# Optimization experiments

Hardware: AMD Instinct MI355X
Metric: run time of the kernel (lower is better)

## Reference

```python
import jax, jax.numpy as jnp
import numpy as np

K = 64          # number of tags, incl. BOS/EOS
V = 50000       # vocab size (excl. BOS/EOS words)
D = 128         # lexicon embedding dim
BOS_T = K - 2   # BOS tag index
EOS_T = K - 1   # EOS tag index
BATCH = 8192
L = 126         # interior words per sentence (n = L + 2 incl. BOS/EOS)
EPS = 1e-45     # smoothing added to A and B in updateAB


def setup_inputs() -> dict:
    key = jax.random.key(0)
    k1, k2, k3, k4 = jax.random.split(key, 4)
    words = jax.random.randint(k1, (BATCH, L), 0, V, dtype=jnp.int32)
    ThetaB = 0.01 * jax.random.uniform(k2, (K, D), dtype=jnp.float32)
    WA = 0.01 * jax.random.uniform(k3, (K, K), dtype=jnp.float32)
    E = jax.random.normal(k4, (V, D), dtype=jnp.float32)
    return {"words": words, "ThetaB": ThetaB, "WA": WA, "E": E}


def reference(words, ThetaB, WA, E):
    # updateAB(): A = softmax(WA) with BOS column forced to prob 0 (-inf logit)
    WAm = WA.at[:, BOS_T].set(-jnp.inf)
    A = jax.nn.softmax(WAm, axis=1) + EPS                       # [K, K]
    B = jax.nn.softmax(ThetaB @ E.T, axis=1)                    # [K, V]
    B = B.at[EOS_T, :].set(0.0).at[BOS_T, :].set(0.0) + EPS
    logA = jnp.log(A)                                           # [K, K]
    logB = jnp.log(B)                                           # [K, V]

    # Emission log-probs gathered per token: [L, B, K]
    em = jnp.swapaxes(logB.T[words], 0, 1)

    # alpha_0: one-hot (in log space) at BOS tag
    alpha0 = jnp.full((words.shape[0], K), -jnp.inf, dtype=logA.dtype)
    alpha0 = alpha0.at[:, BOS_T].set(0.0)

    def step(alpha, e):
        # alpha: [B, K] over prev tags; logsumexp over prev tag axis
        new = jax.nn.logsumexp(alpha[:, :, None] + logA[None, :, :], axis=1) + e
        return new, None

    alpha, _ = jax.lax.scan(step, alpha0, em)
    # Final transition into EOS tag (no emission): log Z per sentence, [B]
    logZ = jax.nn.logsumexp(alpha + logA[None, :, EOS_T], axis=1)
    return logZ
```

## Files before the change

kernel.cpp:

```cpp
#include <hip/hip_runtime.h>
#include <hip/hip_bf16.h>
#include <math.h>


#define KT 64
#define VV 50000
#define DD 128
#define BOS_T 62
#define EOS_T 63
#define LLEN 126
#define EPSF 1e-45f
#define SCALE_F 65536.0f
#define LOG_TOTAL_SCALE (2016.0f * 0.6931471805599453f)
#define NBLK 782
#define PBLK 784
#define PFD 9
#define ROUNDS (LLEN / PFD)

#define BTN_OFF   0
#define A_OFF     3200000
#define SUM_OFF   3216384
#define PART_OFF  3216640

typedef short short8 __attribute__((ext_vector_type(8)));
typedef float f32x4  __attribute__((ext_vector_type(4)));
typedef float f32x2  __attribute__((ext_vector_type(2)));

union U8 { short8 v; unsigned u[4]; short s[8]; };

static __device__ inline unsigned short f2bf_u(float x) {
    __hip_bfloat16 h = __float2bfloat16(x);
    return *reinterpret_cast<unsigned short*>(&h);
}
static __device__ inline short f2bf(float x) { return (short)f2bf_u(x); }

#if __has_builtin(__builtin_amdgcn_cvt_pk_bf16_f32)
typedef __bf16 bf16x2 __attribute__((ext_vector_type(2)));
static __device__ inline unsigned pk2(float a, float b) {
    bf16x2 r = __builtin_amdgcn_cvt_pk_bf16_f32(a, b);
    return *reinterpret_cast<unsigned*>(&r);
}
#else
static __device__ inline unsigned pk2(float a, float b) {
    union { float f; unsigned u; } ua, ub;
    ua.f = a; ub.f = b;
    return ((ua.u + 0x8000u) >> 16) | ((ub.u + 0x8000u) & 0xFFFF0000u);
}
#endif

#if __has_builtin(__builtin_amdgcn_cvt_pk_fp8_f32)
static __device__ inline unsigned pk4f8(float a, float b, float c, float d) {
    int v = __builtin_amdgcn_cvt_pk_fp8_f32(a, b, 0, false);
    v = __builtin_amdgcn_cvt_pk_fp8_f32(c, d, v, true);
    return (unsigned)v;
}
#else
static __device__ inline unsigned enc1f8(float x) {
    union { float f; unsigned u; } c; c.f = x;
    unsigned u = c.u & 0x7FFFFFFFu;
    unsigned r = u + 0x7FFFFu + ((u >> 20) & 1u);
    return ((r >> 20) - (120u << 3)) & 0x7Fu;
}
static __device__ inline unsigned pk4f8(float a, float b, float c, float d) {
    return enc1f8(a) | (enc1f8(b) << 8) | (enc1f8(c) << 16) | (enc1f8(d) << 24);
}
#endif

#if __has_builtin(__builtin_amdgcn_cvt_pk_f32_fp8)
static __device__ inline f32x2 dec2lo(unsigned w) { return __builtin_amdgcn_cvt_pk_f32_fp8((int)w, false); }
static __device__ inline f32x2 dec2hi(unsigned w) { return __builtin_amdgcn_cvt_pk_f32_fp8((int)w, true); }
#else
static __device__ inline float dec1f8(unsigned b) {
    union { unsigned u; float f; } c;
    c.u = ((b & 0x80u) << 24) | (((b & 0x7Fu) << 20) + (120u << 23));
    return c.f;
}
static __device__ inline f32x2 dec2lo(unsigned w) { f32x2 r; r.x = dec1f8(w & 0xFF); r.y = dec1f8((w >> 8) & 0xFF); return r; }
static __device__ inline f32x2 dec2hi(unsigned w) { f32x2 r; r.x = dec1f8((w >> 16) & 0xFF); r.y = dec1f8(w >> 24); return r; }
#endif

__global__ __launch_bounds__(256) void k_emit(const float* __restrict__ ThetaB,
                                              const float* __restrict__ E,
                                              unsigned char* __restrict__ btn8,
                                              float* __restrict__ partial) {
    __shared__ float red[4][KT];
    int t    = threadIdx.x;
    int lane = t & 63;
    int w    = t >> 6;
    int n    = lane & 15;
    int q    = lane >> 4;
    int v0   = (blockIdx.x * 4 + w) * 16;

    int rowE = v0 + n;
    bool valid = rowE < VV;
    rowE = valid ? rowE : VV - 1;
    float4 ex[4][2];
#pragma unroll
    for (int kt = 0; kt < 4; ++kt) {
        const float* p = E + (size_t)rowE * DD + kt * 32 + q * 8;
        ex[kt][0] = *(const float4*)p;
        ex[kt][1] = *(const float4*)(p + 4);
    }

    short8 Th[4][4];
#pragma unroll
    for (int kt = 0; kt < 4; ++kt)
#pragma unroll
        for (int mt = 0; mt < 4; ++mt) {
            const float* p = ThetaB + (mt * 16 + n) * DD + kt * 32 + q * 8;
            float4 x = *(const float4*)p;
            float4 y = *(const float4*)(p + 4);
            U8 f;
            f.u[0] = pk2(x.x, x.y); f.u[1] = pk2(x.z, x.w);
            f.u[2] = pk2(y.x, y.y); f.u[3] = pk2(y.z, y.w);
            Th[kt][mt] = f.v;
        }

    short8 Ef[4];
#pragma unroll
    for (int kt = 0; kt < 4; ++kt) {
        U8 f;
        f.u[0] = pk2(ex[kt][0].x, ex[kt][0].y); f.u[1] = pk2(ex[kt][0].z, ex[kt][0].w);
        f.u[2] = pk2(ex[kt][1].x, ex[kt][1].y); f.u[3] = pk2(ex[kt][1].z, ex[kt][1].w);
        Ef[kt] = f.v;
    }

#pragma unroll
    for (int mt = 0; mt < 4; ++mt) {
        f32x4 C = {0.f, 0.f, 0.f, 0.f};
#pragma unroll
        for (int kt = 0; kt < 4; ++kt)
            C = __builtin_amdgcn_mfma_f32_16x16x32_bf16(Th[kt][mt], Ef[kt], C, 0, 0, 0);
        float e[4];
#pragma unroll
        for (int r = 0; r < 4; ++r) e[r] = __expf(C[r]);
        if (valid) {
            int pos = 16 * ((2 * mt + (q >> 1)) & 3) + 8 * (mt >> 1) + (q & 1) * 4;
            *(unsigned*)(btn8 + (size_t)rowE * KT + pos) = pk4f8(e[0], e[1], e[2], e[3]);
        }
#pragma unroll
        for (int r = 0; r < 4; ++r) {
            float s = valid ? e[r] : 0.0f;
            s += __shfl_xor(s, 1, 64);
            s += __shfl_xor(s, 2, 64);
            s += __shfl_xor(s, 4, 64);
            s += __shfl_xor(s, 8, 64);
            if (n == 0) red[w][mt * 16 + q * 4 + r] = s;
        }
    }
    __syncthreads();
    if (w == 0) {
        float s = red[0][lane] + red[1][lane] + red[2][lane] + red[3][lane];
        partial[lane * PBLK + blockIdx.x] = s;
    }
}

__global__ __launch_bounds__(256) void k_sumA(const float* __restrict__ partial,
                                              const float* __restrict__ WA,
                                              float* __restrict__ sumexp,
                                              float* __restrict__ A) {
    __shared__ float r[4];
    int k = blockIdx.x;
    int t = threadIdx.x;
    float s = 0.0f;
    for (int i = t; i < NBLK; i += 256) s += partial[k * PBLK + i];
#pragma unroll
    for (int off = 32; off > 0; off >>= 1) s += __shfl_xor(s, off, 64);
    if ((t & 63) == 0) r[t >> 6] = s;
    __syncthreads();
    if (t == 0) sumexp[k] = r[0] + r[1] + r[2] + r[3];
    if (t < 64) {
        float wv = WA[k * KT + t];
        float e = (t == BOS_T) ? 0.0f : __expf(wv);
        float se = e;
#pragma unroll
        for (int off = 32; off > 0; off >>= 1) se += __shfl_xor(se, off, 64);
        A[k * KT + t] = e / se + EPSF;
    }
}

__global__ __launch_bounds__(64) void k_scan2(const int* __restrict__ words,
                                              const unsigned char* __restrict__ btn8,
                                              const float* __restrict__ A,
                                              const float* __restrict__ sumexp,
                                              float* __restrict__ out) {
    __shared__ int shw[16 * LLEN];
    int lane = threadIdx.x;
    int n    = lane & 15;
    int qA   = lane >> 4;
    int b0   = blockIdx.x * 16;

    {
        const uint4* src = (const uint4*)(words + (size_t)b0 * LLEN);
        uint4* dst = (uint4*)shw;
#pragma unroll
        for (int it = 0; it < 8; ++it) {
            int idx = it * 64 + lane;
            if (idx < (16 * LLEN) / 4) dst[idx] = src[idx];
        }
    }

    short8 Af[2][4];
#pragma unroll
    for (int mt = 0; mt < 4; ++mt) {
        int tagn = 32 * (mt >> 1) + 8 * (n >> 2) + 4 * (mt & 1) + (n & 3);
        float s = sumexp[tagn];
        float rsn = (tagn == BOS_T || tagn == EOS_T) ? 0.0f : (SCALE_F / s);
#pragma unroll
        for (int kt = 0; kt < 2; ++kt) {
            U8 f;
#pragma unroll
            for (int j = 0; j < 8; ++j)
                f.s[j] = f2bf(A[(kt * 32 + qA * 8 + j) * KT + tagn] * rsn);
            Af[kt][mt] = f.v;
        }
    }
    short8 B0, B1;
    {
        U8 z; z.u[0] = z.u[1] = z.u[2] = z.u[3] = 0;
        B0 = z.v;
        U8 o; o.u[0] = o.u[1] = o.u[2] = o.u[3] = 0;
        if (qA == 3) o.s[6] = (short)0x3F80;
        B1 = o.v;
    }
    __syncthreads();

    const int wrow = n * LLEN;

    uint4 pf[PFD];
    int   wdn[PFD];
#pragma unroll
    for (int j = 0; j < PFD; ++j) {
        int wd = shw[wrow + j];
        pf[j] = *(const uint4*)(btn8 + (size_t)wd * KT + qA * 16);
    }
#pragma unroll
    for (int j = 0; j < PFD; ++j)
        wdn[j] = shw[wrow + PFD + j];

    for (int r = 0; r < ROUNDS; ++r) {
#pragma unroll
        for (int j = 0; j < PFD; ++j) {
            uint4 rc = pf[j];
            pf[j] = *(const uint4*)(btn8 + (size_t)wdn[j] * KT + qA * 16);
            int s18 = r * PFD + j + 2 * PFD;
            s18 = s18 < LLEN ? s18 : LLEN - 1;
            wdn[j] = shw[wrow + s18];

            f32x2 d0 = dec2lo(rc.x), d1 = dec2hi(rc.x);
            f32x2 d2 = dec2lo(rc.y), d3 = dec2hi(rc.y);
            f32x2 d4 = dec2lo(rc.z), d5 = dec2hi(rc.z);
            f32x2 d6 = dec2lo(rc.w), d7 = dec2hi(rc.w);

            f32x4 C[4];
#pragma unroll
            for (int mt = 0; mt < 4; ++mt) {
                f32x4 acc = {0.f, 0.f, 0.f, 0.f};
                acc = __builtin_amdgcn_mfma_f32_16x16x32_bf16(Af[0][mt], B0, acc, 0, 0, 0);
                acc = __builtin_amdgcn_mfma_f32_16x16x32_bf16(Af[1][mt], B1, acc, 0, 0, 0);
                C[mt] = acc;
            }
            U8 f0, f1;
            f0.u[0] = pk2(C[0][0] * d0.x, C[0][1] * d0.y);
            f0.u[1] = pk2(C[0][2] * d1.x, C[0][3] * d1.y);
            f0.u[2] = pk2(C[1][0] * d2.x, C[1][1] * d2.y);
            f0.u[3] = pk2(C[1][2] * d3.x, C[1][3] * d3.y);
            f1.u[0] = pk2(C[2][0] * d4.x, C[2][1] * d4.y);
            f1.u[1] = pk2(C[2][2] * d5.x, C[2][3] * d5.y);
            f1.u[2] = pk2(C[3][0] * d6.x, C[3][1] * d6.y);
            f1.u[3] = pk2(C[3][2] * d7.x, C[3][3] * d7.y);
            B0 = f0.v; B1 = f1.v;
        }
    }

    {
        short8 Afin[2];
#pragma unroll
        for (int kt = 0; kt < 2; ++kt) {
            U8 f;
#pragma unroll
            for (int j = 0; j < 8; ++j)
                f.s[j] = (n == 0) ? f2bf(A[(kt * 32 + qA * 8 + j) * KT + EOS_T]) : (short)0;
            Afin[kt] = f.v;
        }
        f32x4 Cf = {0.f, 0.f, 0.f, 0.f};
        Cf = __builtin_amdgcn_mfma_f32_16x16x32_bf16(Afin[0], B0, Cf, 0, 0, 0);
        Cf = __builtin_amdgcn_mfma_f32_16x16x32_bf16(Afin[1], B1, Cf, 0, 0, 0);
        if (qA == 0)
            out[b0 + n] = logf(Cf[0]) - LOG_TOTAL_SCALE;
    }
}

extern "C" void kernel_launch(void* const* d_in, const int* in_sizes, int n_in,
                              void* d_out, int out_size, void* d_ws, size_t ws_size,
                              hipStream_t stream) {
    const int*   words  = (const int*)d_in[0];
    const float* ThetaB = (const float*)d_in[1];
    const float* WA     = (const float*)d_in[2];
    const float* E      = (const float*)d_in[3];
    float* out = (float*)d_out;

    char* ws = (char*)d_ws;
    unsigned char* btn8 = (unsigned char*)(ws + BTN_OFF);
    float* A       = (float*)(ws + A_OFF);
    float* sumexp  = (float*)(ws + SUM_OFF);
    float* partial = (float*)(ws + PART_OFF);

    k_emit<<<NBLK, 256, 0, stream>>>(ThetaB, E, btn8, partial);
    k_sumA<<<KT, 256, 0, stream>>>(partial, WA, sumexp, A);
    k_scan2<<<8192 / 16, 64, 0, stream>>>(words, btn8, A, sumexp, out);
}
```

Before: 130.0 us.

## Split forward scan into concurrent forward and backward halves per block

```diff
diff --git a/kernel.cpp b/kernel.cpp
--- a/kernel.cpp
+++ b/kernel.cpp
@@ -15,7 +15,8 @@
 #define NBLK 782
 #define PBLK 784
 #define PFD 9
-#define ROUNDS (LLEN / PFD)
+#define HSTEPS 63
+#define HROUNDS (HSTEPS / PFD)
 
 #define BTN_OFF   0
 #define A_OFF     3200000
@@ -33,6 +34,11 @@
     return *reinterpret_cast<unsigned short*>(&h);
 }
 static __device__ inline short f2bf(float x) { return (short)f2bf_u(x); }
+static __device__ inline float bf2f(short s) {
+    union { unsigned u; float f; } c;
+    c.u = ((unsigned)(unsigned short)s) << 16;
+    return c.f;
+}
 
 #if __has_builtin(__builtin_amdgcn_cvt_pk_bf16_f32)
 typedef __bf16 bf16x2 __attribute__((ext_vector_type(2)));
@@ -179,13 +185,18 @@
     }
 }
 
-__global__ __launch_bounds__(64) void k_scan2(const int* __restrict__ words,
-                                              const unsigned char* __restrict__ btn8,
-                                              const float* __restrict__ A,
-                                              const float* __restrict__ sumexp,
-                                              float* __restrict__ out) {
+__global__ __launch_bounds__(128) void k_scan3(const int* __restrict__ words,
+                                               const unsigned char* __restrict__ btn8,
+                                               const float* __restrict__ A,
+                                               const float* __restrict__ sumexp,
+                                               float* __restrict__ out) {
     __shared__ int shw[16 * LLEN];
-    int lane = threadIdx.x;
+    __shared__ float scl[KT];
+    __shared__ float ldx[KT][16];
+    __shared__ float ldy[KT][16];
+    int t    = threadIdx.x;
+    int lane = t & 63;
+    int w    = t >> 6;
     int n    = lane & 15;
     int qA   = lane >> 4;
     int b0   = blockIdx.x * 16;
@@ -193,101 +204,182 @@
     {
         const uint4* src = (const uint4*)(words + (size_t)b0 * LLEN);
         uint4* dst = (uint4*)shw;
-#pragma unroll
-        for (int it = 0; it < 8; ++it) {
-            int idx = it * 64 + lane;
-            if (idx < (16 * LLEN) / 4) dst[idx] = src[idx];
-        }
-    }
-
-    short8 Af[2][4];
-#pragma unroll
-    for (int mt = 0; mt < 4; ++mt) {
-        int tagn = 32 * (mt >> 1) + 8 * (n >> 2) + 4 * (mt & 1) + (n & 3);
-        float s = sumexp[tagn];
-        float rsn = (tagn == BOS_T || tagn == EOS_T) ? 0.0f : (SCALE_F / s);
-#pragma unroll
-        for (int kt = 0; kt < 2; ++kt) {
-            U8 f;
-#pragma unroll
-            for (int j = 0; j < 8; ++j)
-                f.s[j] = f2bf(A[(kt * 32 + qA * 8 + j) * KT + tagn] * rsn);
-            Af[kt][mt] = f.v;
-        }
-    }
-    short8 B0, B1;
-    {
-        U8 z; z.u[0] = z.u[1] = z.u[2] = z.u[3] = 0;
-        B0 = z.v;
-        U8 o; o.u[0] = o.u[1] = o.u[2] = o.u[3] = 0;
-        if (qA == 3) o.s[6] = (short)0x3F80;
-        B1 = o.v;
-    }
+        for (int idx = t; idx < (16 * LLEN) / 4; idx += 128)
+            dst[idx] = src[idx];
+    }
+    if (t < KT)
+        scl[t] = (t == BOS_T || t == EOS_T) ? 0.0f : (SCALE_F / sumexp[t]);
     __syncthreads();
 
     const int wrow = n * LLEN;
 
-    uint4 pf[PFD];
-    int   wdn[PFD];
-#pragma unroll
-    for (int j = 0; j < PFD; ++j) {
-        int wd = shw[wrow + j];
-        pf[j] = *(const uint4*)(btn8 + (size_t)wd * KT + qA * 16);
-    }
-#pragma unroll
-    for (int j = 0; j < PFD; ++j)
-        wdn[j] = shw[wrow + PFD + j];
-
-    for (int r = 0; r < ROUNDS; ++r) {
+    if (w == 0) {
+        short8 Af[2][4];
+#pragma unroll
+        for (int mt = 0; mt < 4; ++mt) {
+            int tagn = 32 * (mt >> 1) + 8 * (n >> 2) + 4 * (mt & 1) + (n & 3);
+            float s = sumexp[tagn];
+            float rsn = (tagn == BOS_T || tagn == EOS_T) ? 0.0f : (SCALE_F / s);
+#pragma unroll
+            for (int kt = 0; kt < 2; ++kt) {
+                U8 f;
+#pragma unroll
+                for (int j = 0; j < 8; ++j)
+                    f.s[j] = f2bf(A[(kt * 32 + qA * 8 + j) * KT + tagn] * rsn);
+                Af[kt][mt] = f.v;
+            }
+        }
+        short8 B0, B1;
+        {
+            U8 z; z.u[0] = z.u[1] = z.u[2] = z.u[3] = 0;
+            B0 = z.v;
+            U8 o; o.u[0] = o.u[1] = o.u[2] = o.u[3] = 0;
+            if (qA == 3) o.s[6] = (short)0x3F80;
+            B1 = o.v;
+        }
+
+        uint4 pf[PFD];
+        int   wdn[PFD];
 #pragma unroll
         for (int j = 0; j < PFD; ++j) {
-            uint4 rc = pf[j];
-            pf[j] = *(const uint4*)(btn8 + (size_t)wdn[j] * KT + qA * 16);
-            int s18 = r * PFD + j + 2 * PFD;
-            s18 = s18 < LLEN ? s18 : LLEN - 1;
-            wdn[j] = shw[wrow + s18];
-
-            f32x2 d0 = dec2lo(rc.x), d1 = dec2hi(rc.x);
-            f32x2 d2 = dec2lo(rc.y), d3 = dec2hi(rc.y);
-            f32x2 d4 = dec2lo(rc.z), d5 = dec2hi(rc.z);
-            f32x2 d6 = dec2lo(rc.w), d7 = dec2hi(rc.w);
-
-            f32x4 C[4];
-#pragma unroll
-            for (int mt = 0; mt < 4; ++mt) {
-                f32x4 acc = {0.f, 0.f, 0.f, 0.f};
-                acc = __builtin_amdgcn_mfma_f32_16x16x32_bf16(Af[0][mt], B0, acc, 0, 0, 0);
-                acc = __builtin_amdgcn_mfma_f32_16x16x32_bf16(Af[1][mt], B1, acc, 0, 0, 0);
-                C[mt] = acc;
-            }
-            U8 f0, f1;
-            f0.u[0] = pk2(C[0][0] * d0.x, C[0][1] * d0.y);
-            f0.u[1] = pk2(C[0][2] * d1.x, C[0][3] * d1.y);
-            f0.u[2] = pk2(C[1][0] * d2.x, C[1][1] * d2.y);
-            f0.u[3] = pk2(C[1][2] * d3.x, C[1][3] * d3.y);
-            f1.u[0] = pk2(C[2][0] * d4.x, C[2][1] * d4.y);
-            f1.u[1] = pk2(C[2][2] * d5.x, C[2][3] * d5.y);
-            f1.u[2] = pk2(C[3][0] * d6.x, C[3][1] * d6.y);
-            f1.u[3] = pk2(C[3][2] * d7.x, C[3][3] * d7.y);
-            B0 = f0.v; B1 = f1.v;
-        }
-    }
-
-    {
-        short8 Afin[2];
-#pragma unroll
-        for (int kt = 0; kt < 2; ++kt) {
-            U8 f;
-#pragma unroll
-            for (int j = 0; j < 8; ++j)
-                f.s[j] = (n == 0) ? f2bf(A[(kt * 32 + qA * 8 + j) * KT + EOS_T]) : (short)0;
-            Afin[kt] = f.v;
-        }
-        f32x4 Cf = {0.f, 0.f, 0.f, 0.f};
-        Cf = __builtin_amdgcn_mfma_f32_16x16x32_bf16(Afin[0], B0, Cf, 0, 0, 0);
-        Cf = __builtin_amdgcn_mfma_f32_16x16x32_bf16(Afin[1], B1, Cf, 0, 0, 0);
+            int wd = shw[wrow + j];
+            pf[j] = *(const uint4*)(btn8 + (size_t)wd * KT + qA * 16);
+        }
+#pragma unroll
+        for (int j = 0; j < PFD; ++j)
+            wdn[j] = shw[wrow + PFD + j];
+
+        for (int r = 0; r < HROUNDS; ++r) {
+#pragma unroll
+            for (int j = 0; j < PFD; ++j) {
+                uint4 rc = pf[j];
+                pf[j] = *(const uint4*)(btn8 + (size_t)wdn[j] * KT + qA * 16);
+                int s18 = r * PFD + j + 2 * PFD;
+                s18 = s18 < HSTEPS ? s18 : HSTEPS - 1;
+                wdn[j] = shw[wrow + s18];
+
+                f32x2 d0 = dec2lo(rc.x), d1 = dec2hi(rc.x);
+                f32x2 d2 = dec2lo(rc.y), d3 = dec2hi(rc.y);
+                f32x2 d4 = dec2lo(rc.z), d5 = dec2hi(rc.z);
+                f32x2 d6 = dec2lo(rc.w), d7 = dec2hi(rc.w);
+
+                f32x4 C[4];
+#pragma unroll
+                for (int mt = 0; mt < 4; ++mt) {
+                    f32x4 acc = {0.f, 0.f, 0.f, 0.f};
+                    acc = __builtin_amdgcn_mfma_f32_16x16x32_bf16(Af[0][mt], B0, acc, 0, 0, 0);
+                    acc = __builtin_amdgcn_mfma_f32_16x16x32_bf16(Af[1][mt], B1, acc, 0, 0, 0);
+                    C[mt] = acc;
+                }
+                U8 f0, f1;
+                f0.u[0] = pk2(C[0][0] * d0.x, C[0][1] * d0.y);
+                f0.u[1] = pk2(C[0][2] * d1.x, C[0][3] * d1.y);
+                f0.u[2] = pk2(C[1][0] * d2.x, C[1][1] * d2.y);
+                f0.u[3] = pk2(C[1][2] * d3.x, C[1][3] * d3.y);
+                f1.u[0] = pk2(C[2][0] * d4.x, C[2][1] * d4.y);
+                f1.u[1] = pk2(C[2][2] * d5.x, C[2][3] * d5.y);
+                f1.u[2] = pk2(C[3][0] * d6.x, C[3][1] * d6.y);
+                f1.u[3] = pk2(C[3][2] * d7.x, C[3][3] * d7.y);
+                B0 = f0.v; B1 = f1.v;
+            }
+        }
+        U8 bx0, bx1; bx0.v = B0; bx1.v = B1;
+#pragma unroll
+        for (int j = 0; j < 8; ++j) {
+            ldx[qA * 8 + j][n]      = bf2f(bx0.s[j]);
+            ldx[32 + qA * 8 + j][n] = bf2f(bx1.s[j]);
+        }
+    } else {
+        short8 Af[2][4];
+#pragma unroll
+        for (int mt = 0; mt < 4; ++mt) {
+            int tagn = 32 * (mt >> 1) + 8 * (n >> 2) + 4 * (mt & 1) + (n & 3);
+#pragma unroll
+            for (int kt = 0; kt < 2; ++kt) {
+                U8 f;
+#pragma unroll
+                for (int j = 0; j < 8; ++j) {
+                    int kc = kt * 32 + qA * 8 + j;
+                    f.s[j] = f2bf(A[tagn * KT + kc] * scl[kc]);
+                }
+                Af[kt][mt] = f.v;
+            }
+        }
+        f32x4 C[4];
+#pragma unroll
+        for (int mt = 0; mt < 4; ++mt)
+#pragma unroll
+            for (int r = 0; r < 4; ++r) {
+                int tg = 32 * (mt >> 1) + 8 * qA + 4 * (mt & 1) + r;
+                C[mt][r] = A[tg * KT + EOS_T];
+            }
+
+        uint4 pf[PFD];
+        int   wdn[PFD];
+#pragma unroll
+        for (int j = 0; j < PFD; ++j) {
+            int wd = shw[wrow + (LLEN - 1 - j)];
+            pf[j] = *(const uint4*)(btn8 + (size_t)wd * KT + qA * 16);
+        }
+#pragma unroll
+        for (int j = 0; j < PFD; ++j)
+            wdn[j] = shw[wrow + (LLEN - 1 - (PFD + j))];
+
+        for (int r = 0; r < HROUNDS; ++r) {
+#pragma unroll
+            for (int j = 0; j < PFD; ++j) {
+                uint4 rc = pf[j];
+                pf[j] = *(const uint4*)(btn8 + (size_t)wdn[j] * KT + qA * 16);
+                int itn = r * PFD + j + 2 * PFD;
+                itn = itn < HSTEPS ? itn : HSTEPS - 1;
+                wdn[j] = shw[wrow + (LLEN - 1 - itn)];
+
+                f32x2 d0 = dec2lo(rc.x), d1 = dec2hi(rc.x);
+                f32x2 d2 = dec2lo(rc.y), d3 = dec2hi(rc.y);
+                f32x2 d4 = dec2lo(rc.z), d5 = dec2hi(rc.z);
+                f32x2 d6 = dec2lo(rc.w), d7 = dec2hi(rc.w);
+
+                U8 f0, f1;
+                f0.u[0] = pk2(C[0][0] * d0.x, C[0][1] * d0.y);
+                f0.u[1] = pk2(C[0][2] * d1.x, C[0][3] * d1.y);
+                f0.u[2] = pk2(C[1][0] * d2.x, C[1][1] * d2.y);
+                f0.u[3] = pk2(C[1][2] * d3.x, C[1][3] * d3.y);
+                f1.u[0] = pk2(C[2][0] * d4.x, C[2][1] * d4.y);
+                f1.u[1] = pk2(C[2][2] * d5.x, C[2][3] * d5.y);
+                f1.u[2] = pk2(C[3][0] * d6.x, C[3][1] * d6.y);
+                f1.u[3] = pk2(C[3][2] * d7.x, C[3][3] * d7.y);
+                short8 B0 = f0.v, B1 = f1.v;
+
+#pragma unroll
+                for (int mt = 0; mt < 4; ++mt) {
+                    f32x4 acc = {0.f, 0.f, 0.f, 0.f};
+                    acc = __builtin_amdgcn_mfma_f32_16x16x32_bf16(Af[0][mt], B0, acc, 0, 0, 0);
+                    acc = __builtin_amdgcn_mfma_f32_16x16x32_bf16(Af[1][mt], B1, acc, 0, 0, 0);
+                    C[mt] = acc;
+                }
+            }
+        }
+#pragma unroll
+        for (int mt = 0; mt < 4; ++mt)
+#pragma unroll
+            for (int r = 0; r < 4; ++r) {
+                int tg = 32 * (mt >> 1) + 8 * qA + 4 * (mt & 1) + r;
+                ldy[tg][n] = C[mt][r];
+            }
+    }
+    __syncthreads();
+
+    if (w == 0) {
+        float s = 0.0f;
+#pragma unroll
+        for (int kk = 0; kk < 16; ++kk) {
+            int tg = qA * 16 + kk;
+            s += ldx[tg][n] * ldy[tg][n];
+        }
+        s += __shfl_xor(s, 16, 64);
+        s += __shfl_xor(s, 32, 64);
         if (qA == 0)
-            out[b0 + n] = logf(Cf[0]) - LOG_TOTAL_SCALE;
+            out[b0 + n] = logf(s) - LOG_TOTAL_SCALE;
     }
 }
 
@@ -308,5 +400,5 @@
 
     k_emit<<<NBLK, 256, 0, stream>>>(ThetaB, E, btn8, partial);
     k_sumA<<<KT, 256, 0, stream>>>(partial, WA, sumexp, A);
-    k_scan2<<<8192 / 16, 64, 0, stream>>>(words, btn8, A, sumexp, out);
-}
+    k_scan3<<<8192 / 16, 128, 0, stream>>>(words, btn8, A, sumexp, out);
+}
```

After: 125.2 us. -3.7%, faster.
